# Performance work log

Hardware: AMD Instinct MI355X
Metric: run time of the kernel (lower is better)

## Reference

```python
import jax, jax.numpy as jnp
import numpy as np

H = 768   # encoder hidden size
NH = 4    # boundary attention heads
HD = H // NH
E = 9     # ent_type_size
R = 12    # rel_type_size
D = 64    # inner_dim
B = 4
S = 1024


def setup_inputs() -> dict:
    key = jax.random.key(0)
    ks = jax.random.split(key, 8)
    n = lambda k, shp: jax.random.normal(k, shp, jnp.float32) * 0.02
    return dict(
        hidden_states=jax.random.normal(ks[0], (B, S, H), jnp.float32),
        attention_mask=jnp.ones((B, S), jnp.float32),
        in_proj_w=n(ks[1], (3 * H, H)), in_proj_b=jnp.zeros((3 * H,), jnp.float32),
        out_proj_w=n(ks[2], (H, H)), out_proj_b=jnp.zeros((H,), jnp.float32),
        gate_w=n(ks[3], (H, H)), gate_b=jnp.zeros((H,), jnp.float32),
        ln_g=jnp.ones((H,), jnp.float32), ln_b=jnp.zeros((H,), jnp.float32),
        ent_w=n(ks[4], (E * 2 * D, H)), ent_b=jnp.zeros((E * 2 * D,), jnp.float32),
        prior_w=n(ks[5], (H, E)), prior_b=jnp.zeros((H,), jnp.float32),
        rel_w=n(ks[6], (R * 2 * D, 2 * H)), rel_b=jnp.zeros((R * 2 * D,), jnp.float32),
    )


def _sinusoidal_pos_emb(seq_len, dim, dtype):
    pos = jnp.arange(seq_len, dtype=dtype)[:, None]                 # [S,1]
    inv = jnp.power(jnp.asarray(10000.0, dtype), -2.0 * jnp.arange(dim // 2, dtype=dtype) / dim)
    ang = pos * inv                                                  # [S,D/2]
    emb = jnp.stack([jnp.sin(ang), jnp.cos(ang)], axis=-1).reshape(seq_len, dim)  # [sin0,cos0,sin1,cos1,...]
    return emb


def _gp_matrix(hs, W, b, mask):
    # hs: [B,S,Hin], W: [T*2D, Hin], mask: [B,S]
    bsz, seq_len, _ = hs.shape
    out = hs @ W.T + b                                               # [B,S,T*2D]
    T = out.shape[-1] // (2 * D)
    out = out.reshape(bsz, seq_len, T, 2 * D)
    qw, kw = out[..., :D], out[..., D:]                              # [B,S,T,D]
    # RoPE
    pe = _sinusoidal_pos_emb(seq_len, D, hs.dtype)                   # [S,D]
    cos = jnp.repeat(pe[:, 1::2], 2, axis=-1)[None, :, None, :]      # [1,S,1,D]
    sin = jnp.repeat(pe[:, ::2], 2, axis=-1)[None, :, None, :]

    def rot(x):
        x2 = jnp.stack([-x[..., 1::2], x[..., ::2]], axis=-1).reshape(x.shape)
        return x * cos + x2 * sin

    qw, kw = rot(qw), rot(kw)
    logits = jnp.einsum('bmtd,bntd->btmn', qw, kw)                   # [B,T,S,S]
    pad = mask[:, None, None, :]                                     # masks key dim
    logits = logits * pad - (1.0 - pad) * 1e12
    tril = jnp.tril(jnp.ones((seq_len, seq_len), logits.dtype), -1)
    logits = logits - tril * 1e12                                    # strictly lower triangle masked
    return logits / jnp.sqrt(jnp.asarray(D, logits.dtype))


def _boundary_attention(hs, mask, in_proj_w, in_proj_b, out_proj_w, out_proj_b,
                        gate_w, gate_b, ln_g, ln_b):
    bsz, seq_len, _ = hs.shape
    qkv = hs @ in_proj_w.T + in_proj_b                               # [B,S,3H]
    q, k, v = jnp.split(qkv, 3, axis=-1)
    q = q.reshape(bsz, seq_len, NH, HD)
    k = k.reshape(bsz, seq_len, NH, HD)
    v = v.reshape(bsz, seq_len, NH, HD)
    scores = jnp.einsum('bqhd,bkhd->bhqk', q, k) / jnp.sqrt(jnp.asarray(HD, hs.dtype))
    key_pad = (mask == 0)[:, None, None, :]                          # [B,1,1,S]
    scores = jnp.where(key_pad, jnp.asarray(-1e9, hs.dtype), scores)
    attn = jax.nn.softmax(scores, axis=-1)
    ctx = jnp.einsum('bhqk,bkhd->bqhd', attn, v).reshape(bsz, seq_len, H)
    attn_out = ctx @ out_proj_w.T + out_proj_b
    gate = jax.nn.sigmoid(attn_out @ gate_w.T + gate_b)
    x = hs + gate * attn_out
    mu = jnp.mean(x, axis=-1, keepdims=True)
    var = jnp.var(x, axis=-1, keepdims=True)
    return (x - mu) / jnp.sqrt(var + 1e-5) * ln_g + ln_b


def reference(hidden_states, attention_mask, in_proj_w, in_proj_b, out_proj_w, out_proj_b,
              gate_w, gate_b, ln_g, ln_b, ent_w, ent_b, prior_w, prior_b, rel_w, rel_b):
    enhanced = _boundary_attention(hidden_states, attention_mask, in_proj_w, in_proj_b,
                                   out_proj_w, out_proj_b, gate_w, gate_b, ln_g, ln_b)
    ent_logits = _gp_matrix(enhanced, ent_w, ent_b, attention_mask)  # [B,E,S,S]
    ent_prior = jnp.max(ent_logits, axis=-1)                          # [B,E,S]
    ent_prior = jnp.swapaxes(ent_prior, 1, 2)                         # [B,S,E]
    prior_feat = jax.nn.relu(ent_prior @ prior_w.T + prior_b)         # [B,S,H]
    rel_hidden = jnp.concatenate([enhanced, prior_feat], axis=-1)     # [B,S,2H]
    rel_logits = _gp_matrix(rel_hidden, rel_w, rel_b, attention_mask) # [B,R,S,S]
    return (ent_logits, rel_logits, enhanced)
```

## Files before the change

kernel.cpp:

```cpp
#include <hip/hip_runtime.h>
#include <math.h>

#define H_   768
#define NH_  4
#define HD_  192
#define E_   9
#define R_   12
#define D_   64
#define B_   4
#define S_   1024
#define H3_  (3 * H_)
#define MBS_ (B_ * S_)

typedef unsigned short u16;
typedef __attribute__((ext_vector_type(4))) int   i32x4;
typedef __attribute__((ext_vector_type(4))) float f32x4;
typedef __attribute__((ext_vector_type(8))) unsigned short u16x8;

static const long OUT_REL_OFF = (long)B_ * E_ * S_ * S_;
static const long OUT_ENH_OFF = OUT_REL_OFF + (long)B_ * R_ * S_ * S_;

__device__ __forceinline__ u16 f2bf(float f) {
    unsigned u = __builtin_bit_cast(unsigned, f);
    return (u16)((u + 0x7fffu + ((u >> 16) & 1u)) >> 16);
}
__device__ __forceinline__ float bf2f(u16 h) {
    return __builtin_bit_cast(float, (unsigned)h << 16);
}
__device__ __forceinline__ void gload16(const u16* g, u16* l) {
    __builtin_amdgcn_global_load_lds(
        (__attribute__((address_space(1))) void*)g,
        (__attribute__((address_space(3))) void*)l, 16, 0, 0);
}
__device__ __forceinline__ void mfma_bf16(f32x4& acc, i32x4 a, i32x4 b) {
    asm volatile("v_mfma_f32_16x16x32_bf16 %0, %1, %2, %0"
                 : "+v"(acc) : "v"(a), "v"(b));
}

template<int BM, int BN, int EPI, int OBF>
__global__ __launch_bounds__(256) void gemm_mfma(
    const u16* __restrict__ A, const u16* __restrict__ Bw,
    const float* __restrict__ bias, void* __restrict__ Cv,
    int K, int lda, int ldb, int ldc, int nh,
    long sAb, long sAh, long sBb, long sBh, long sCb, long sCh,
    const float* __restrict__ mask, float scale, float* __restrict__ aux)
{
    constexpr int MI = BM / 32, NJ = BN / 32;
    const int z = blockIdx.z;
    const int zb = z / nh, zh = z - zb * nh;
    A  += zb * sAb + zh * sAh;
    Bw += zb * sBb + zh * sBh;

    const int gx = gridDim.x, gy = gridDim.y;
    int id = blockIdx.y * gx + blockIdx.x;
    const int nwg = gx * gy;
    if ((nwg & 7) == 0) id = (id & 7) * (nwg >> 3) + (id >> 3);
    const int bx = id % gx, by = id / gx;
    const int m0 = by * BM, n0 = bx * BN;

    __shared__ u16 lds[(BM + BN) * 64];
    __shared__ float sminv[BM];
    u16* ldsA = lds;
    u16* ldsB = lds + BM * 64;

    const int t = threadIdx.x;
    const int lane = t & 63, wid = t >> 6;
    const int wr = wid >> 1, wc = wid & 1;
    const int l16 = lane & 15, l4 = lane >> 4;

    f32x4 acc[MI][NJ];
    #pragma unroll
    for (int mi = 0; mi < MI; ++mi)
        #pragma unroll
        for (int nj = 0; nj < NJ; ++nj)
            #pragma unroll
            for (int q = 0; q < 4; ++q) acc[mi][nj][q] = 0.0f;

    for (int k0 = 0; k0 < K; k0 += 64) {
        #pragma unroll
        for (int i = 0; i < BM / 32; ++i) {
            const int e = i * 256 + t;
            const int row = e >> 3;
            const int c = ((e & 7) ^ (row & 7)) << 3;
            gload16(A + (long)(m0 + row) * lda + k0 + c, ldsA + e * 8);
        }
        #pragma unroll
        for (int i = 0; i < BN / 32; ++i) {
            const int e = i * 256 + t;
            const int row = e >> 3;
            const int c = ((e & 7) ^ (row & 7)) << 3;
            gload16(Bw + (long)(n0 + row) * ldb + k0 + c, ldsB + e * 8);
        }
        __syncthreads();
        i32x4 af[MI][2], bfr[NJ][2];
        #pragma unroll
        for (int mi = 0; mi < MI; ++mi)
            #pragma unroll
            for (int kk = 0; kk < 2; ++kk) {
                const int row = wr * (BM / 2) + mi * 16 + l16;
                af[mi][kk] = *(const i32x4*)&ldsA[row * 64 + ((((kk << 2) + l4) ^ (row & 7)) << 3)];
            }
        #pragma unroll
        for (int nj = 0; nj < NJ; ++nj)
            #pragma unroll
            for (int kk = 0; kk < 2; ++kk) {
                const int row = wc * (BN / 2) + nj * 16 + l16;
                bfr[nj][kk] = *(const i32x4*)&ldsB[row * 64 + ((((kk << 2) + l4) ^ (row & 7)) << 3)];
            }
        #pragma unroll
        for (int kk = 0; kk < 2; ++kk)
            #pragma unroll
            for (int mi = 0; mi < MI; ++mi)
                #pragma unroll
                for (int nj = 0; nj < NJ; ++nj)
                    mfma_bf16(acc[mi][nj], af[mi][kk], bfr[nj][kk]);
        __syncthreads();
    }
    __builtin_amdgcn_sched_barrier(0);
    asm volatile("s_nop 7");
    asm volatile("s_nop 7");
    __builtin_amdgcn_sched_barrier(0);

    if (EPI == 1 || EPI == 3 || EPI == 5) mask += (long)zb * S_;
    const long cbase = zb * sCb + zh * sCh;

    if (EPI == 6) {
        if (t < BM) {
            const float* pp = aux + ((long)z * S_ + m0 + t) * 16;
            float s = 0.0f;
            #pragma unroll
            for (int i = 0; i < 16; ++i) s += pp[i];
            sminv[t] = 1.0f / s;
        }
        __syncthreads();
    }

    float red[MI][4];
    if (EPI == 3 || EPI == 5) {
        #pragma unroll
        for (int mi = 0; mi < MI; ++mi)
            #pragma unroll
            for (int r = 0; r < 4; ++r) red[mi][r] = (EPI == 3) ? -INFINITY : 0.0f;
    }

    #pragma unroll
    for (int mi = 0; mi < MI; ++mi) {
        #pragma unroll
        for (int nj = 0; nj < NJ; ++nj) {
            const int gn = n0 + wc * (BN / 2) + nj * 16 + l16;
            const float bv = ((EPI == 0 || EPI == 4) && bias) ? bias[gn] : 0.0f;
            float invf = 0.0f;
            if (EPI == 4) invf = exp2f(-(float)((gn & 63) >> 1) * 0.41524101186092503f);
            #pragma unroll
            for (int r = 0; r < 4; ++r) {
                const int gm = m0 + wr * (BM / 2) + mi * 16 + l4 * 4 + r;
                float v = acc[mi][nj][r];
                const long cidx = cbase + (long)gm * ldc + gn;
                if (EPI == 0) {
                    v += bv;
                    if (OBF) ((u16*)Cv)[cidx] = f2bf(v);
                    else     ((float*)Cv)[cidx] = v;
                } else if (EPI == 1 || EPI == 3) {
                    const float pad = mask[gn];
                    v = v * pad - (1.0f - pad) * 1e12f;
                    if (gm > gn) v -= 1e12f;
                    v *= 0.125f;
                    ((float*)Cv)[cidx] = v;
                    if (EPI == 3) red[mi][r] = fmaxf(red[mi][r], v);
                } else if (EPI == 5) {
                    float tv = 0.0f;
                    if (mask[gn] != 0.0f) tv = __expf(v * scale);
                    ((u16*)Cv)[cidx] = f2bf(tv);
                    red[mi][r] += tv;
                } else if (EPI == 6) {
                    v *= sminv[gm - m0];
                    ((u16*)Cv)[cidx] = f2bf(v);
                } else {
                    v += bv;
                    const int sp = gm & (S_ - 1);
                    float sn, cs;
                    __sincosf((float)sp * invf, &sn, &cs);
                    const float pv = __shfl_xor(v, 1, 64);
                    v = (gn & 1) ? fmaf(v, cs, pv * sn) : fmaf(v, cs, -pv * sn);
                    ((u16*)Cv)[cidx] = f2bf(v);
                }
            }
        }
    }

    if (EPI == 3 || EPI == 5) {
        #pragma unroll
        for (int mi = 0; mi < MI; ++mi) {
            #pragma unroll
            for (int r = 0; r < 4; ++r) {
                float m = red[mi][r];
                if (EPI == 3) {
                    m = fmaxf(m, __shfl_xor(m, 1, 64));
                    m = fmaxf(m, __shfl_xor(m, 2, 64));
                    m = fmaxf(m, __shfl_xor(m, 4, 64));
                    m = fmaxf(m, __shfl_xor(m, 8, 64));
                } else {
                    m += __shfl_xor(m, 1, 64);
                    m += __shfl_xor(m, 2, 64);
                    m += __shfl_xor(m, 4, 64);
                    m += __shfl_xor(m, 8, 64);
                }
                if (l16 == 0) {
                    const int gm = m0 + wr * (BM / 2) + mi * 16 + l4 * 4 + r;
                    aux[((long)z * S_ + gm) * 16 + bx * 2 + wc] = m;
                }
            }
        }
    }
}

__global__ __launch_bounds__(256) void cast_all(
    const float* __restrict__ hs, const float* __restrict__ ipw,
    const float* __restrict__ opw, const float* __restrict__ gw,
    const float* __restrict__ entw, const float* __restrict__ relw,
    u16* hs_o, u16* ipw_o, u16* opw_o, u16* gw_o, u16* entw_o, u16* relw_o)
{
    const int blk = blockIdx.x;
    const float* in; u16* out; long base;
    if      (blk < 3072) { in = hs;   out = hs_o;   base = (long)blk * 1024; }
    else if (blk < 4800) { in = ipw;  out = ipw_o;  base = (long)(blk - 3072) * 1024; }
    else if (blk < 5376) { in = opw;  out = opw_o;  base = (long)(blk - 4800) * 1024; }
    else if (blk < 5952) { in = gw;   out = gw_o;   base = (long)(blk - 5376) * 1024; }
    else if (blk < 6816) { in = entw; out = entw_o; base = (long)(blk - 5952) * 1024; }
    else                 { in = relw; out = relw_o; base = (long)(blk - 6816) * 1024; }
    const long idx = base + (long)threadIdx.x * 4;
    const float4 v = *(const float4*)&in[idx];
    ushort4 o; o.x = f2bf(v.x); o.y = f2bf(v.y); o.z = f2bf(v.z); o.w = f2bf(v.w);
    *(ushort4*)&out[idx] = o;
}

__global__ __launch_bounds__(256) void transpose_v(
    const u16* __restrict__ qkv, u16* __restrict__ vt)
{
    __shared__ u16 tile[64][72];
    const int z = blockIdx.z, b = z >> 2, h = z & 3;
    const int d0 = blockIdx.x * 64, s0 = blockIdx.y * 64;
    const int t = threadIdx.x;
    const int r = t >> 2, c = (t & 3) << 4;
    const u16* src = qkv + ((long)(b * S_ + s0 + r)) * H3_ + 2 * H_ + h * HD_ + d0 + c;
    *(u16x8*)&tile[r][c]     = *(const u16x8*)src;
    *(u16x8*)&tile[r][c + 8] = *(const u16x8*)(src + 8);
    __syncthreads();
    u16 tmp[16];
    #pragma unroll
    for (int i = 0; i < 16; ++i) tmp[i] = tile[c + i][r];
    u16* dst = vt + ((long)z * HD_ + d0 + r) * S_ + s0 + c;
    *(u16x8*)dst       = *(u16x8*)&tmp[0];
    *(u16x8*)(dst + 8) = *(u16x8*)&tmp[8];
}

__global__ __launch_bounds__(256) void gate_ln_bf(
    const float* __restrict__ hs, const u16* __restrict__ aogl,
    const float* __restrict__ g, const float* __restrict__ bta,
    float* __restrict__ enh, u16* __restrict__ relh)
{
    const long row = blockIdx.x;
    const float* hrow = hs + row * H_;
    const u16* arow = aogl + row * (2 * H_);
    const int tid = threadIdx.x;
    float x[3];
    float sum = 0.0f, sq = 0.0f;
    #pragma unroll
    for (int i = 0; i < 3; ++i) {
        const int j = tid + i * 256;
        const float a = bf2f(arow[j]);
        const float gt = 1.0f / (1.0f + __expf(-bf2f(arow[H_ + j])));
        const float xv = hrow[j] + gt * a;
        x[i] = xv; sum += xv; sq += xv * xv;
    }
    __shared__ float sm[8];
    #pragma unroll
    for (int o = 32; o > 0; o >>= 1) {
        sum += __shfl_xor(sum, o, 64);
        sq  += __shfl_xor(sq, o, 64);
    }
    const int lane = tid & 63, wid = tid >> 6;
    if (lane == 0) { sm[wid] = sum; sm[4 + wid] = sq; }
    __syncthreads();
    sum = sm[0] + sm[1] + sm[2] + sm[3];
    sq  = sm[4] + sm[5] + sm[6] + sm[7];
    const float mu = sum * (1.0f / (float)H_);
    float var = sq * (1.0f / (float)H_) - mu * mu;
    var = fmaxf(var, 0.0f);
    const float inv = 1.0f / sqrtf(var + 1e-5f);
    #pragma unroll
    for (int i = 0; i < 3; ++i) {
        const int j = tid + i * 256;
        const float o = (x[i] - mu) * inv * g[j] + bta[j];
        enh[row * H_ + j] = o;
        relh[row * (2 * H_) + j] = f2bf(o);
    }
}

__global__ __launch_bounds__(256) void prior_fused(
    const float* __restrict__ pmax, const float* __restrict__ pw,
    const float* __restrict__ pb, u16* __restrict__ relh)
{
    const int row = blockIdx.x;
    const int b = row >> 10, m = row & (S_ - 1);
    __shared__ float pr[E_];
    const int tid = threadIdx.x;
    if (tid < E_) {
        const float* pp = pmax + ((long)(b * E_ + tid) * S_ + m) * 16;
        float mx = -INFINITY;
        #pragma unroll
        for (int i = 0; i < 16; ++i) mx = fmaxf(mx, pp[i]);
        pr[tid] = mx;
    }
    __syncthreads();
    float p[E_];
    #pragma unroll
    for (int e = 0; e < E_; ++e) p[e] = pr[e];
    u16* orow = relh + (long)row * (2 * H_) + H_;
    #pragma unroll
    for (int i = 0; i < 3; ++i) {
        const int j = tid + i * 256;
        float a = pb[j];
        #pragma unroll
        for (int e = 0; e < E_; ++e) a = fmaf(p[e], pw[j * E_ + e], a);
        orow[j] = f2bf(fmaxf(a, 0.0f));
    }
}

extern "C" void kernel_launch(void* const* d_in, const int* in_sizes, int n_in,
                              void* d_out, int out_size, void* d_ws, size_t ws_size,
                              hipStream_t stream)
{
    const float* hs   = (const float*)d_in[0];
    const float* mask = (const float*)d_in[1];
    const float* ipw  = (const float*)d_in[2];
    const float* ipb  = (const float*)d_in[3];
    const float* opw  = (const float*)d_in[4];
    const float* opb  = (const float*)d_in[5];
    const float* gw   = (const float*)d_in[6];
    const float* gb   = (const float*)d_in[7];
    const float* lng  = (const float*)d_in[8];
    const float* lnb  = (const float*)d_in[9];
    const float* entw = (const float*)d_in[10];
    const float* entb = (const float*)d_in[11];
    const float* prw  = (const float*)d_in[12];
    const float* prb  = (const float*)d_in[13];
    const float* relw = (const float*)d_in[14];
    const float* relb = (const float*)d_in[15];
    float* out = (float*)d_out;
    char* base = (char*)d_ws;

    u16* ipw_bf  = (u16*)(base + 0);
    u16* opw_bf  = (u16*)(base + 3538944);
    u16* gw_bf   = (u16*)(base + 4718592);
    u16* entw_bf = (u16*)(base + 5898240);
    u16* relw_bf = (u16*)(base + 7667712);
    u16* hs_bf   = (u16*)(base + 12386304);
    u16* qkv_bf  = (u16*)(base + 18677760);
    u16* vt_bf   = (u16*)(base + 37552128);
    u16* sc_bf   = (u16*)(base + 43843584);
    u16* ctx_bf  = (u16*)(base + 77398016);
    u16* aogl_bf = (u16*)(base + 83689472);
    float* bias2 = (float*)(base + 96272384);
    float* psum  = (float*)(base + 96280576);
    float* pmax  = (float*)(base + 97329152);
    u16* relh_bf = (u16*)(base + 18677760);
    u16* projr   = (u16*)(base + 37552128);
    float* enh   = out + OUT_ENH_OFF;

    const float qscale = 0.07216878364870323f;

    hipMemcpyAsync(bias2, opb, H_ * sizeof(float), hipMemcpyDeviceToDevice, stream);
    hipMemcpyAsync(bias2 + H_, gb, H_ * sizeof(float), hipMemcpyDeviceToDevice, stream);

    cast_all<<<9120, 256, 0, stream>>>(hs, ipw, opw, gw, entw, relw,
                                       hs_bf, ipw_bf, opw_bf, gw_bf, entw_bf, relw_bf);

    gemm_mfma<128,128,0,1><<<dim3(18, 32, 1), 256, 0, stream>>>(
        hs_bf, ipw_bf, ipb, qkv_bf, H_, H_, H_, H3_, 1,
        0,0,0,0,0,0, nullptr, 0.0f, nullptr);

    transpose_v<<<dim3(3, 16, 16), 256, 0, stream>>>(qkv_bf, vt_bf);

    gemm_mfma<128,128,5,1><<<dim3(8, 8, B_ * NH_), 256, 0, stream>>>(
        qkv_bf, qkv_bf + H_, nullptr, sc_bf, HD_, H3_, H3_, S_, NH_,
        (long)S_ * H3_, HD_, (long)S_ * H3_, HD_,
        (long)NH_ * S_ * S_, (long)S_ * S_, mask, qscale, psum);

    gemm_mfma<128,64,6,1><<<dim3(3, 8, B_ * NH_), 256, 0, stream>>>(
        sc_bf, vt_bf, nullptr, ctx_bf, S_, S_, S_, H_, NH_,
        (long)NH_ * S_ * S_, (long)S_ * S_, (long)NH_ * HD_ * S_, (long)HD_ * S_,
        (long)S_ * H_, HD_, nullptr, 0.0f, psum);

    gemm_mfma<128,128,0,1><<<dim3(12, 32, 1), 256, 0, stream>>>(
        ctx_bf, opw_bf, bias2, aogl_bf, H_, H_, H_, 2 * H_, 1,
        0,0,0,0,0,0, nullptr, 0.0f, nullptr);

    gate_ln_bf<<<MBS_, 256, 0, stream>>>(hs, aogl_bf, lng, lnb, enh, relh_bf);

    gemm_mfma<128,128,4,1><<<dim3(9, 32, 1), 256, 0, stream>>>(
        relh_bf, entw_bf, entb, projr, H_, 2 * H_, H_, E_ * 2 * D_, 1,
        0,0,0,0,0,0, nullptr, 0.0f, nullptr);

    gemm_mfma<128,128,3,0><<<dim3(8, 8, B_ * E_), 256, 0, stream>>>(
        projr, projr + D_, nullptr, out, D_, E_ * 2 * D_, E_ * 2 * D_, S_, E_,
        (long)S_ * E_ * 2 * D_, 2 * D_, (long)S_ * E_ * 2 * D_, 2 * D_,
        (long)E_ * S_ * S_, (long)S_ * S_, mask, 0.0f, pmax);

    prior_fused<<<MBS_, 256, 0, stream>>>(pmax, prw, prb, relh_bf);

    gemm_mfma<128,128,4,1><<<dim3(12, 32, 1), 256, 0, stream>>>(
        relh_bf, relw_bf, relb, projr, 2 * H_, 2 * H_, 2 * H_, R_ * 2 * D_, 1,
        0,0,0,0,0,0, nullptr, 0.0f, nullptr);

    gemm_mfma<128,128,1,0><<<dim3(8, 8, B_ * R_), 256, 0, stream>>>(
        projr, projr + D_, nullptr, out + OUT_REL_OFF, D_, R_ * 2 * D_, R_ * 2 * D_, S_, R_,
        (long)S_ * R_ * 2 * D_, 2 * D_, (long)S_ * R_ * 2 * D_, 2 * D_,
        (long)R_ * S_ * S_, (long)S_ * S_, mask, 0.0f, nullptr);

    (void)in_sizes; (void)n_in; (void)out_size; (void)ws_size;
}
```

Measured before the change: 252.8 us.

## Double-buffer LDS tiles in MFMA GEMM to overlap global loads with compute

```diff
diff --git a/kernel.cpp b/kernel.cpp
--- a/kernel.cpp
+++ b/kernel.cpp
@@ -37,7 +37,7 @@
                  : "+v"(acc) : "v"(a), "v"(b));
 }
 
-template<int BM, int BN, int EPI, int OBF>
+template<int BM, int BN, int EPI, int OBF, int NS>
 __global__ __launch_bounds__(256) void gemm_mfma(
     const u16* __restrict__ A, const u16* __restrict__ Bw,
     const float* __restrict__ bias, void* __restrict__ Cv,
@@ -46,6 +46,7 @@
     const float* __restrict__ mask, float scale, float* __restrict__ aux)
 {
     constexpr int MI = BM / 32, NJ = BN / 32;
+    constexpr int BUFE = (BM + BN) * 64;
     const int z = blockIdx.z;
     const int zb = z / nh, zh = z - zb * nh;
     A  += zb * sAb + zh * sAh;
@@ -58,54 +59,63 @@
     const int bx = id % gx, by = id / gx;
     const int m0 = by * BM, n0 = bx * BN;
 
-    __shared__ u16 lds[(BM + BN) * 64];
-    __shared__ float sminv[BM];
-    u16* ldsA = lds;
-    u16* ldsB = lds + BM * 64;
+    __shared__ u16 lds[NS * BUFE];
 
     const int t = threadIdx.x;
     const int lane = t & 63, wid = t >> 6;
     const int wr = wid >> 1, wc = wid & 1;
     const int l16 = lane & 15, l4 = lane >> 4;
 
-    f32x4 acc[MI][NJ];
-    #pragma unroll
-    for (int mi = 0; mi < MI; ++mi)
-        #pragma unroll
-        for (int nj = 0; nj < NJ; ++nj)
-            #pragma unroll
-            for (int q = 0; q < 4; ++q) acc[mi][nj][q] = 0.0f;
-
-    for (int k0 = 0; k0 < K; k0 += 64) {
+    auto stage = [&](int kt, int buf) {
+        u16* la = lds + buf * BUFE;
+        u16* lb = la + BM * 64;
+        const int k0 = kt << 6;
         #pragma unroll
         for (int i = 0; i < BM / 32; ++i) {
             const int e = i * 256 + t;
             const int row = e >> 3;
             const int c = ((e & 7) ^ (row & 7)) << 3;
-            gload16(A + (long)(m0 + row) * lda + k0 + c, ldsA + e * 8);
+            gload16(A + (long)(m0 + row) * lda + k0 + c, la + e * 8);
         }
         #pragma unroll
         for (int i = 0; i < BN / 32; ++i) {
             const int e = i * 256 + t;
             const int row = e >> 3;
             const int c = ((e & 7) ^ (row & 7)) << 3;
-            gload16(Bw + (long)(n0 + row) * ldb + k0 + c, ldsB + e * 8);
+            gload16(Bw + (long)(n0 + row) * ldb + k0 + c, lb + e * 8);
         }
-        __syncthreads();
+    };
+
+    f32x4 acc[MI][NJ];
+    #pragma unroll
+    for (int mi = 0; mi < MI; ++mi)
+        #pragma unroll
+        for (int nj = 0; nj < NJ; ++nj)
+            #pragma unroll
+            for (int q = 0; q < 4; ++q) acc[mi][nj][q] = 0.0f;
+
+    const int nt = K >> 6;
+    stage(0, 0);
+    __syncthreads();
+    for (int tt = 0; tt < nt; ++tt) {
+        const int cur = (NS == 2) ? (tt & 1) : 0;
+        if (NS == 2 && tt + 1 < nt) stage(tt + 1, cur ^ 1);
+        const u16* la = lds + cur * BUFE;
+        const u16* lb = la + BM * 64;
         i32x4 af[MI][2], bfr[NJ][2];
         #pragma unroll
         for (int mi = 0; mi < MI; ++mi)
             #pragma unroll
             for (int kk = 0; kk < 2; ++kk) {
                 const int row = wr * (BM / 2) + mi * 16 + l16;
-                af[mi][kk] = *(const i32x4*)&ldsA[row * 64 + ((((kk << 2) + l4) ^ (row & 7)) << 3)];
+                af[mi][kk] = *(const i32x4*)&la[row * 64 + ((((kk << 2) + l4) ^ (row & 7)) << 3)];
             }
         #pragma unroll
         for (int nj = 0; nj < NJ; ++nj)
             #pragma unroll
             for (int kk = 0; kk < 2; ++kk) {
                 const int row = wc * (BN / 2) + nj * 16 + l16;
-                bfr[nj][kk] = *(const i32x4*)&ldsB[row * 64 + ((((kk << 2) + l4) ^ (row & 7)) << 3)];
+                bfr[nj][kk] = *(const i32x4*)&lb[row * 64 + ((((kk << 2) + l4) ^ (row & 7)) << 3)];
             }
         #pragma unroll
         for (int kk = 0; kk < 2; ++kk)
@@ -124,6 +134,7 @@
     if (EPI == 1 || EPI == 3 || EPI == 5) mask += (long)zb * S_;
     const long cbase = zb * sCb + zh * sCh;
 
+    float* sminv = (float*)lds;
     if (EPI == 6) {
         if (t < BM) {
             const float* pp = aux + ((long)z * S_ + m0 + t) * 16;
@@ -376,44 +387,44 @@
     cast_all<<<9120, 256, 0, stream>>>(hs, ipw, opw, gw, entw, relw,
                                        hs_bf, ipw_bf, opw_bf, gw_bf, entw_bf, relw_bf);
 
-    gemm_mfma<128,128,0,1><<<dim3(18, 32, 1), 256, 0, stream>>>(
+    gemm_mfma<128,128,0,1,2><<<dim3(18, 32, 1), 256, 0, stream>>>(
         hs_bf, ipw_bf, ipb, qkv_bf, H_, H_, H_, H3_, 1,
         0,0,0,0,0,0, nullptr, 0.0f, nullptr);
 
     transpose_v<<<dim3(3, 16, 16), 256, 0, stream>>>(qkv_bf, vt_bf);
 
-    gemm_mfma<128,128,5,1><<<dim3(8, 8, B_ * NH_), 256, 0, stream>>>(
+    gemm_mfma<128,128,5,1,2><<<dim3(8, 8, B_ * NH_), 256, 0, stream>>>(
         qkv_bf, qkv_bf + H_, nullptr, sc_bf, HD_, H3_, H3_, S_, NH_,
         (long)S_ * H3_, HD_, (long)S_ * H3_, HD_,
         (long)NH_ * S_ * S_, (long)S_ * S_, mask, qscale, psum);
 
-    gemm_mfma<128,64,6,1><<<dim3(3, 8, B_ * NH_), 256, 0, stream>>>(
+    gemm_mfma<128,64,6,1,2><<<dim3(3, 8, B_ * NH_), 256, 0, stream>>>(
         sc_bf, vt_bf, nullptr, ctx_bf, S_, S_, S_, H_, NH_,
         (long)NH_ * S_ * S_, (long)S_ * S_, (long)NH_ * HD_ * S_, (long)HD_ * S_,
         (long)S_ * H_, HD_, nullptr, 0.0f, psum);
 
-    gemm_mfma<128,128,0,1><<<dim3(12, 32, 1), 256, 0, stream>>>(
+    gemm_mfma<128,128,0,1,2><<<dim3(12, 32, 1), 256, 0, stream>>>(
         ctx_bf, opw_bf, bias2, aogl_bf, H_, H_, H_, 2 * H_, 1,
         0,0,0,0,0,0, nullptr, 0.0f, nullptr);
 
     gate_ln_bf<<<MBS_, 256, 0, stream>>>(hs, aogl_bf, lng, lnb, enh, relh_bf);
 
-    gemm_mfma<128,128,4,1><<<dim3(9, 32, 1), 256, 0, stream>>>(
+    gemm_mfma<128,128,4,1,2><<<dim3(9, 32, 1), 256, 0, stream>>>(
         relh_bf, entw_bf, entb, projr, H_, 2 * H_, H_, E_ * 2 * D_, 1,
         0,0,0,0,0,0, nullptr, 0.0f, nullptr);
 
-    gemm_mfma<128,128,3,0><<<dim3(8, 8, B_ * E_), 256, 0, stream>>>(
+    gemm_mfma<128,128,3,0,1><<<dim3(8, 8, B_ * E_), 256, 0, stream>>>(
         projr, projr + D_, nullptr, out, D_, E_ * 2 * D_, E_ * 2 * D_, S_, E_,
         (long)S_ * E_ * 2 * D_, 2 * D_, (long)S_ * E_ * 2 * D_, 2 * D_,
         (long)E_ * S_ * S_, (long)S_ * S_, mask, 0.0f, pmax);
 
     prior_fused<<<MBS_, 256, 0, stream>>>(pmax, prw, prb, relh_bf);
 
-    gemm_mfma<128,128,4,1><<<dim3(12, 32, 1), 256, 0, stream>>>(
+    gemm_mfma<128,128,4,1,2><<<dim3(12, 32, 1), 256, 0, stream>>>(
         relh_bf, relw_bf, relb, projr, 2 * H_, 2 * H_, 2 * H_, R_ * 2 * D_, 1,
         0,0,0,0,0,0, nullptr, 0.0f, nullptr);
 
-    gemm_mfma<128,128,1,0><<<dim3(8, 8, B_ * R_), 256, 0, stream>>>(
+    gemm_mfma<128,128,1,0,1><<<dim3(8, 8, B_ * R_), 256, 0, stream>>>(
         projr, projr + D_, nullptr, out + OUT_REL_OFF, D_, R_ * 2 * D_, R_ * 2 * D_, S_, R_,
         (long)S_ * R_ * 2 * D_, 2 * D_, (long)S_ * R_ * 2 * D_, 2 * D_,
         (long)R_ * S_ * S_, (long)S_ * S_, mask, 0.0f, nullptr);
```

Result: no change. 256.4 us (+1.4%).
